# Kernel tuning notes

Hardware: AMD Instinct MI355X
Metric: run time of the kernel (lower is better)

## Reference

```python
import jax, jax.numpy as jnp
import numpy as np

WIN = (4, 16)
HEADS = 4
DIM = 128
HID = 512

def _rel_index(win):
    ch = np.arange(win[0]); cw = np.arange(win[1])
    coords = np.stack(np.meshgrid(ch, cw, indexing='ij')).reshape(2, -1)  # 2, N
    rel = (coords[:, :, None] - coords[:, None, :]).transpose(1, 2, 0).astype(np.int64)  # N,N,2
    rel[:, :, 0] += win[0] - 1
    rel[:, :, 1] += win[1] - 1
    rel[:, :, 0] *= 2 * win[1] - 1
    return jnp.asarray(rel.sum(-1))  # (N, N) int

REL_IDX = _rel_index(WIN)

def _ln(x, g, b):
    m = x.mean(-1, keepdims=True)
    v = ((x - m) ** 2).mean(-1, keepdims=True)
    return (x - m) / jnp.sqrt(v + 1e-5) * g + b

def _gelu(x):
    return jax.nn.gelu(x, approximate=False)

def _posconv3d(x, w, b):
    # depthwise 3x3x3 conv with singleton depth axis; x: B,C,H,W; w: C,1,3,3,3
    y = jax.lax.conv_general_dilated(x[:, :, None], w, (1, 1, 1), ((1, 1), (1, 1), (1, 1)),
                                     feature_group_count=x.shape[1],
                                     dimension_numbers=('NCDHW', 'OIDHW', 'NCDHW'))
    return y[:, :, 0] + b[None, :, None, None]

def _dwconv2d(x, w, b):
    # depthwise 3x3 conv; x: B,Ch,H,W; w: Ch,1,3,3
    y = jax.lax.conv_general_dilated(x, w, (1, 1), ((1, 1), (1, 1)),
                                     feature_group_count=x.shape[1],
                                     dimension_numbers=('NCHW', 'OIHW', 'NCHW'))
    return y + b[None, :, None, None]

def setup_inputs() -> dict:
    key = jax.random.key(0)
    ks = jax.random.split(key, 12)
    B, C, H, W = 4, DIM, 192, 192
    s = 0.02
    return {
        'x': jax.random.normal(ks[0], (B, C, H, W), jnp.float32),
        'pos_w': jax.random.normal(ks[1], (C, 1, 3, 3, 3), jnp.float32) * s,
        'pos_b': jnp.zeros((C,), jnp.float32),
        'ln1_g': jnp.ones((C,), jnp.float32),
        'ln1_b': jnp.zeros((C,), jnp.float32),
        'q_w': jax.random.normal(ks[2], (C, C), jnp.float32) * s,
        'q_b': jnp.zeros((C,), jnp.float32),
        'kv_w': jax.random.normal(ks[3], (C, 2 * C), jnp.float32) * s,
        'kv_b': jnp.zeros((2 * C,), jnp.float32),
        'rpb': jax.random.normal(ks[4], ((2 * WIN[0] - 1) * (2 * WIN[1] - 1), HEADS), jnp.float32) * s,
        'proj_w': jax.random.normal(ks[5], (C, C), jnp.float32) * s,
        'proj_b': jnp.zeros((C,), jnp.float32),
        'fft1_w': jax.random.normal(ks[6], (2 * C, 2 * C), jnp.float32) * s,
        'fft1_b': jnp.zeros((2 * C,), jnp.float32),
        'fft2_w': jax.random.normal(ks[7], (2 * C, 2 * C), jnp.float32) * s,
        'fft2_b': jnp.zeros((2 * C,), jnp.float32),
        'ln2_g': jnp.ones((C,), jnp.float32),
        'ln2_b': jnp.zeros((C,), jnp.float32),
        'l1_w': jax.random.normal(ks[8], (C, HID), jnp.float32) * s,
        'l1_b': jnp.zeros((HID,), jnp.float32),
        'dw_w': jax.random.normal(ks[9], (HID, 1, 3, 3), jnp.float32) * s,
        'dw_b': jnp.zeros((HID,), jnp.float32),
        'l2_w': jax.random.normal(ks[10], (HID, C), jnp.float32) * s,
        'l2_b': jnp.zeros((C,), jnp.float32),
    }

def _forward(x, pos_w, pos_b, ln1_g, ln1_b, q_w, q_b, kv_w, kv_b, rpb, proj_w, proj_b,
             fft1_w, fft1_b, fft2_w, fft2_b, ln2_g, ln2_b, l1_w, l1_b, dw_w, dw_b, l2_w, l2_b):
    B, C, H, W = x.shape
    wh, ww = WIN
    N = wh * ww
    hd = C // HEADS
    # depthwise 3D positional embedding
    x = x + _posconv3d(x, pos_w, pos_b)
    xt = x.transpose(0, 2, 3, 1)  # B,H,W,C
    shortcut = xt
    xn = _ln(xt, ln1_g, ln1_b)
    # window partition: (B*nW, N, C)  (idx=0 -> no shift, no mask)
    win = xn.reshape(B, H // wh, wh, W // ww, ww, C).transpose(0, 1, 3, 2, 4, 5).reshape(-1, N, C)
    q = (win @ q_w + q_b).reshape(-1, N, HEADS, hd).transpose(0, 2, 1, 3)  # Bw,h,N,d
    kv = (win @ kv_w + kv_b).reshape(-1, N, 2, HEADS, hd).transpose(2, 0, 3, 1, 4)
    k, v = kv[0], kv[1]
    attn = jnp.einsum('bhnd,bhmd->bhnm', q * (hd ** -0.5), k)
    rel_bias = rpb[REL_IDX].transpose(2, 0, 1)  # heads,N,N
    attn = jax.nn.softmax(attn + rel_bias[None], axis=-1)
    out = jnp.einsum('bhnm,bhmd->bhnd', attn, v).transpose(0, 2, 1, 3).reshape(-1, N, C)
    out = out @ proj_w + proj_b
    out = out.reshape(B, H // wh, W // ww, wh, ww, C).transpose(0, 1, 3, 2, 4, 5).reshape(B, H, W, C)
    xt = shortcut + out
    # FFT residual branch (two 1x1 convs on cat(real,imag))
    xc = xt.transpose(0, 3, 1, 2)  # B,C,H,W
    f = jnp.fft.rfft2(xc, axes=(-2, -1))
    ff = jnp.concatenate([f.real, f.imag], axis=1)  # B,2C,H,Wf
    ff = jnp.einsum('bchw,co->bohw', ff, fft1_w) + fft1_b[None, :, None, None]
    ff = jnp.where(ff >= 0, ff, 0.01 * ff)  # LeakyReLU(0.01)
    ff = jnp.einsum('bchw,co->bohw', ff, fft2_w) + fft2_b[None, :, None, None]
    fr, fi = jnp.split(ff, 2, axis=1)
    y = jnp.fft.irfft2(fr + 1j * fi, s=(H, W), axes=(-2, -1))
    xt = xt + y.transpose(0, 2, 3, 1)
    # LeFF: linear -> dwconv -> linear, on full (H,W) grid
    xn2 = _ln(xt, ln2_g, ln2_b)
    h1 = _gelu(xn2 @ l1_w + l1_b)               # B,H,W,HID
    h1 = _gelu(_dwconv2d(h1.transpose(0, 3, 1, 2), dw_w, dw_b))
    h2 = h1.transpose(0, 2, 3, 1) @ l2_w + l2_b  # B,H,W,C
    xt = xt + h2
    return xt.transpose(0, 3, 1, 2)

def reference(x, pos_w, pos_b, ln1_g, ln1_b, q_w, q_b, kv_w, kv_b, rpb, proj_w, proj_b,
              fft1_w, fft1_b, fft2_w, fft2_b, ln2_g, ln2_b, l1_w, l1_b, dw_w, dw_b, l2_w, l2_b):
    return _forward(x, pos_w, pos_b, ln1_g, ln1_b, q_w, q_b, kv_w, kv_b, rpb, proj_w, proj_b,
                    fft1_w, fft1_b, fft2_w, fft2_b, ln2_g, ln2_b, l1_w, l1_b, dw_w, dw_b, l2_w, l2_b)
```

## Files before the change

### kernel.cpp

```cpp
#include <hip/hip_runtime.h>
#include <hip/hip_bf16.h>
#include <math.h>

#define C_DIM 128
#define HGT 192
#define WID 192
#define NB 4
#define WFD 97

#define T_BIAS  0
#define T_QKVB  16384
#define TF_SZ   16896
#define UT_MW    0
#define UT_MHF   49152
#define UT_MHI   196608
#define UT_MWI   344064
#define UT_QKVW  387072
#define UT_PROJW 436224
#define UT_FFT1W 452608
#define UT_FFT2W 518144
#define UT_L1W   583680
#define UT_L2W   649216
#define UT_TOT   714752
#define TAB_SZ   374272

typedef __attribute__((ext_vector_type(8))) short bf16x8;
typedef __attribute__((ext_vector_type(4))) float f32x4;

__device__ __forceinline__ float gelu_f(float v){
  return 0.5f*v*(1.0f + erff(v*0.70710678118654752440f));
}
__device__ __forceinline__ unsigned short f2bf(float f){
  __hip_bfloat16 h = __float2bfloat16(f);
  return *reinterpret_cast<unsigned short*>(&h);
}
__device__ __forceinline__ float bf2f(unsigned short u){
  unsigned int x = ((unsigned int)u)<<16;
  return __uint_as_float(x);
}
__device__ __forceinline__ void st8u(unsigned short* d, bf16x8 v){
  unsigned int* wp = (unsigned int*)&v;
  unsigned int* dp = (unsigned int*)d;
  dp[0]=wp[0]; dp[1]=wp[1]; dp[2]=wp[2]; dp[3]=wp[3];
}

__global__ __launch_bounds__(256) void build_tables(float* __restrict__ tab,
        const float* __restrict__ rpb, const float* __restrict__ q_b, const float* __restrict__ kv_b,
        const float* __restrict__ q_w, const float* __restrict__ kv_w, const float* __restrict__ proj_w,
        const float* __restrict__ fft1_w, const float* __restrict__ fft2_w,
        const float* __restrict__ l1_w, const float* __restrict__ l2_w){
  int idx = blockIdx.x*256 + threadIdx.x;
  const float STEP = (float)(6.283185307179586476925286766559/192.0);
  if (idx < 16384){
    int head = idx>>12, n = (idx>>6)&63, m = idx&63;
    int dh = n/16 - m/16 + 3;
    int dw = (n&15) - (m&15) + 15;
    tab[T_BIAS+idx] = rpb[(dh*31+dw)*4 + head];
    return;
  }
  idx -= 16384;
  if (idx < 384){
    tab[T_QKVB+idx] = (idx < 128) ? q_b[idx] : kv_b[idx-128];
    return;
  }
  idx -= 384;
  unsigned short* ut = (unsigned short*)(tab + TF_SZ);
  if (idx < 49152){
    int r = idx/192, w = idx%192;
    float v = 0.f;
    if (r < 97){ int a = (r*w)%192; v = cosf(a*STEP); }
    else if (r < 194){ int a = ((r-97)*w)%192; v = -sinf(a*STEP); }
    ut[UT_MW+idx] = f2bf(v);
    return;
  }
  idx -= 49152;
  if (idx < 147456){
    int r = idx/384, j = idx%384;
    int hf = (r < 192) ? r : r-192;
    int h  = (j < 192) ? j : j-192;
    int a = (hf*h)%192;
    float c = cosf(a*STEP), s = sinf(a*STEP);
    float v;
    if (r < 192) v = (j < 192) ? c : s;
    else         v = (j < 192) ? -s : c;
    ut[UT_MHF+idx] = f2bf(v);
    return;
  }
  idx -= 147456;
  if (idx < 147456){
    int r = idx/384, j = idx%384;
    int h  = (r < 192) ? r : r-192;
    int hf = (j < 192) ? j : j-192;
    int a = (h*hf)%192;
    float c = cosf(a*STEP), s = sinf(a*STEP);
    float v;
    if (r < 192) v = (j < 192) ? c : -s;
    else         v = (j < 192) ? s : c;
    ut[UT_MHI+idx] = f2bf(v);
    return;
  }
  idx -= 147456;
  if (idx < 43008){
    int w = idx/224, j = idx%224;
    float v = 0.f;
    if (j < 97){
      int a = (j*w)%192;
      float sc = ((j==0 || j==96) ? 1.f : 2.f) / 36864.f;
      v = sc*cosf(a*STEP);
    } else if (j >= 112 && j < 209){
      int k = j-112;
      int a = (k*w)%192;
      float sc = ((k==0 || k==96) ? 1.f : 2.f) / 36864.f;
      v = -sc*sinf(a*STEP);
    }
    ut[UT_MWI+idx] = f2bf(v);
    return;
  }
  idx -= 43008;
  if (idx < 49152){
    int n = idx/128, k = idx%128;
    float v = (n < 128) ? q_w[(size_t)k*128 + n] : kv_w[(size_t)k*256 + (n-128)];
    ut[UT_QKVW+idx] = f2bf(v);
    return;
  }
  idx -= 49152;
  if (idx < 16384){
    int n = idx/128, k = idx%128;
    ut[UT_PROJW+idx] = f2bf(proj_w[(size_t)k*128 + n]);
    return;
  }
  idx -= 16384;
  if (idx < 65536){
    int n = idx/256, k = idx%256;
    ut[UT_FFT1W+idx] = f2bf(fft1_w[(size_t)k*256 + n]);
    return;
  }
  idx -= 65536;
  if (idx < 65536){
    int n = idx/256, k = idx%256;
    ut[UT_FFT2W+idx] = f2bf(fft2_w[(size_t)k*256 + n]);
    return;
  }
  idx -= 65536;
  if (idx < 65536){
    int n = idx/128, k = idx%128;
    ut[UT_L1W+idx] = f2bf(l1_w[(size_t)k*512 + n]);
    return;
  }
  idx -= 65536;
  if (idx < 65536){
    int n = idx/512, k = idx%512;
    ut[UT_L2W+idx] = f2bf(l2_w[(size_t)k*128 + n]);
  }
}

__global__ __launch_bounds__(256) void posconv3_kernel(const float* __restrict__ x, const float* __restrict__ pw,
                               const float* __restrict__ pb, float* __restrict__ xt){
  __shared__ float rows_s[16*340];
  int w0 = blockIdx.x*32, h0 = blockIdx.y*8;
  int b = blockIdx.z >> 3, cb = (blockIdx.z & 7)*16;
  int tid = threadIdx.x;
  int hl = tid >> 5, wl = tid & 31;
  for (int e = tid; e < 16*340; e += 256){
    int c = e / 340; int rem = e - c*340;
    int r = rem / 34; int wc = rem - r*34;
    int gh = h0 - 1 + r, gw = w0 - 1 + wc;
    float v = 0.f;
    if (gh >= 0 && gh < HGT && gw >= 0 && gw < WID)
      v = x[((size_t)(b*C_DIM + cb + c))*(HGT*WID) + gh*WID + gw];
    rows_s[e] = v;
  }
  __syncthreads();
  float outr[16];
  #pragma unroll
  for (int c = 0; c < 16; ++c){
    const float* rs = &rows_s[c*340];
    float wreg[9];
    #pragma unroll
    for (int t9 = 0; t9 < 9; ++t9) wreg[t9] = pw[(cb+c)*27 + 9 + t9];
    float bias = pb[cb+c];
    float acc = rs[(hl+1)*34 + wl+1] + bias;
    #pragma unroll
    for (int ky = 0; ky < 3; ++ky)
      #pragma unroll
      for (int kx = 0; kx < 3; ++kx)
        acc += wreg[ky*3+kx]*rs[(hl+ky)*34 + wl+kx];
    outr[c] = acc;
  }
  __syncthreads();
  {
    int px = hl*32 + wl;
    #pragma unroll
    for (int c = 0; c < 16; ++c) rows_s[px*17 + c] = outr[c];
  }
  __syncthreads();
  for (int r = 0; r < 16; ++r){
    int e = r*256 + tid;
    int cl = e & 15, hw = e >> 4;
    int h = hw >> 5, w = hw & 31;
    xt[((size_t)(b*HGT + h0+h)*WID + (w0+w))*C_DIM + cb + cl] = rows_s[hw*17 + cl];
  }
}

__global__ __launch_bounds__(256) void ln_stats_kernel(const float* __restrict__ src, float* __restrict__ stats){
  int wave = threadIdx.x >> 6; int lane = threadIdx.x & 63;
  size_t p = (size_t)blockIdx.x*4 + wave;
  const float* s = src + p*C_DIM;
  float v0 = s[lane], v1 = s[lane+64];
  float sum = v0 + v1;
  #pragma unroll
  for (int o=1; o<64; o<<=1) sum += __shfl_xor(sum, o, 64);
  float m = sum * (1.0f/128.0f);
  float d0 = v0-m, d1 = v1-m;
  float vs = d0*d0 + d1*d1;
  #pragma unroll
  for (int o=1; o<64; o<<=1) vs += __shfl_xor(vs, o, 64);
  float rstd = rsqrtf(vs*(1.0f/128.0f) + 1e-5f);
  if (lane==0){ stats[2*p] = m; stats[2*p+1] = rstd; }
}

template<int ACT, bool ADD, bool LNA, bool ABF, bool OBF, int NT>
__global__ __launch_bounds__(256) void gemm2(const void* __restrict__ A1v,
                            const unsigned short* __restrict__ WT, const float* __restrict__ bias,
                            void* __restrict__ dstv, int K, int N, int lda,
                            const float* __restrict__ stats, const float* __restrict__ lng,
                            const float* __restrict__ lnb, int prow0, int pmax){
  __shared__ __align__(16) unsigned short As[64*40];
  __shared__ __align__(16) unsigned short Bs[NT][64*40];
  int p0 = blockIdx.y*64, n00 = blockIdx.x*(64*NT);
  int tid = threadIdx.x;
  int wave = tid >> 6, lane = tid & 63;
  int wr = (wave>>1)*32, wc = (wave&1)*32;
  f32x4 acc[NT][4];
  #pragma unroll
  for (int nt=0; nt<NT; ++nt)
    #pragma unroll
    for (int q=0; q<4; ++q) acc[nt][q] = (f32x4){};
  int am = tid >> 2, ak = (tid & 3)*8;
  int brow = tid >> 2, bkk = (tid & 3)*8;
  for (int k0 = 0; k0 < K; k0 += 32){
    if constexpr (ABF){
      const unsigned short* A1u = (const unsigned short*)A1v;
      bf16x8 av = *(const bf16x8*)(A1u + (size_t)(p0+am)*lda + k0 + ak);
      st8u(&As[am*40 + ak], av);
    } else {
      int gp = p0 + am;
      float s0 = 0.f, s1 = 0.f;
      if (LNA){
        gp += prow0;
        gp = gp < 0 ? 0 : (gp > pmax ? pmax : gp);
        s0 = stats[2*gp]; s1 = stats[2*gp+1];
      }
      const float* src = (const float*)A1v + (size_t)gp*lda + k0 + ak;
      float4 aa = *(const float4*)src;
      float4 ab = *(const float4*)(src+4);
      float v[8] = {aa.x,aa.y,aa.z,aa.w,ab.x,ab.y,ab.z,ab.w};
      unsigned short* dp = &As[am*40 + ak];
      #pragma unroll
      for (int j=0;j<8;j++){
        float f = v[j];
        if (LNA) f = (f - s0)*s1*lng[k0+ak+j] + lnb[k0+ak+j];
        dp[j] = f2bf(f);
      }
    }
    #pragma unroll
    for (int nt=0; nt<NT; ++nt){
      bf16x8 wv = *(const bf16x8*)(WT + (size_t)(n00 + nt*64 + brow)*K + k0 + bkk);
      st8u(&Bs[nt][brow*40 + bkk], wv);
    }
    __syncthreads();
    int fm = lane & 15, kg = (lane>>4)*8;
    bf16x8 a0 = *(const bf16x8*)&As[(wr+fm)*40 + kg];
    bf16x8 a1 = *(const bf16x8*)&As[(wr+16+fm)*40 + kg];
    #pragma unroll
    for (int nt=0; nt<NT; ++nt){
      bf16x8 b0 = *(const bf16x8*)&Bs[nt][(wc+fm)*40 + kg];
      bf16x8 b1 = *(const bf16x8*)&Bs[nt][(wc+16+fm)*40 + kg];
      acc[nt][0] = __builtin_amdgcn_mfma_f32_16x16x32_bf16(a0, b0, acc[nt][0], 0,0,0);
      acc[nt][1] = __builtin_amdgcn_mfma_f32_16x16x32_bf16(a0, b1, acc[nt][1], 0,0,0);
      acc[nt][2] = __builtin_amdgcn_mfma_f32_16x16x32_bf16(a1, b0, acc[nt][2], 0,0,0);
      acc[nt][3] = __builtin_amdgcn_mfma_f32_16x16x32_bf16(a1, b1, acc[nt][3], 0,0,0);
    }
    __syncthreads();
  }
  int cn = lane & 15, rq = (lane>>4)*4;
  #pragma unroll
  for (int nt=0; nt<NT; ++nt){
    #pragma unroll
    for (int mi=0; mi<2; ++mi){
      #pragma unroll
      for (int ni=0; ni<2; ++ni){
        f32x4 a = acc[nt][mi*2+ni];
        int n = n00 + nt*64 + wc + ni*16 + cn;
        float bsv = bias[n];
        #pragma unroll
        for (int r=0; r<4; ++r){
          size_t row = (size_t)p0 + wr + mi*16 + rq + r;
          float v = a[r] + bsv;
          if (ACT==1) v = (v>=0.f) ? v : 0.01f*v;
          if (ACT==2) v = gelu_f(v);
          if constexpr (OBF){
            ((unsigned short*)dstv)[row*(size_t)N + n] = f2bf(v);
          } else {
            float* dst = (float*)dstv;
            if (ADD) v += dst[row*(size_t)N + n];
            dst[row*(size_t)N + n] = v;
          }
        }
      }
    }
  }
}

template<int MODE>
__global__ __launch_bounds__(256) void dft_gemm(const unsigned short* __restrict__ Atab,
                            const void* __restrict__ W1v, const void* __restrict__ W2v,
                            void* __restrict__ D1v, void* __restrict__ D2v, int k0){
  constexpr int K      = (MODE==0)?192 : (MODE==3)?224 : 384;
  constexpr int MT     = (MODE==0)?4 : (MODE==3)?3 : 6;
  constexpr int MVALID = (MODE==0)?194 : (MODE==3)?192 : 384;
  __shared__ __align__(16) unsigned short As[64*40];
  __shared__ __align__(16) unsigned short Bs[64*40];
  int slab = blockIdx.y / MT;
  int p0 = (blockIdx.y % MT)*64, n0 = blockIdx.x*64;
  int tid = threadIdx.x;
  int wave = tid >> 6, lane = tid & 63;
  int wr = (wave>>1)*32, wc = (wave&1)*32;
  f32x4 acc00 = {}, acc01 = {}, acc10 = {}, acc11 = {};
  int am = tid >> 2, ak = (tid & 3)*8;
  int bk = tid >> 3, bn = (tid & 7)*8;
  for (int kk0 = 0; kk0 < K; kk0 += 32){
    {
      bf16x8 av = *(const bf16x8*)(Atab + (size_t)(p0+am)*K + kk0 + ak);
      st8u(&As[am*40 + ak], av);
    }
    {
      int r = kk0 + bk;
      if (MODE==0){
        const float* src = (const float*)W1v + (size_t)slab*24576 + (size_t)r*128 + n0 + bn;
        float4 wa = *(const float4*)src;
        float4 wb = *(const float4*)(src+4);
        float v[8] = {wa.x,wa.y,wa.z,wa.w,wb.x,wb.y,wb.z,wb.w};
        #pragma unroll
        for (int j=0;j<8;j++) Bs[(bn+j)*40 + bk] = f2bf(v[j]);
      } else {
        const unsigned short* src;
        if (MODE==1) src = (r<192) ? (const unsigned short*)W1v + (size_t)(k0+slab)*128 + (size_t)r*12416
                                   : (const unsigned short*)W2v + (size_t)(k0+slab)*128 + (size_t)(r-192)*12416;
        else if (MODE==2) src = (r<192) ? (const unsigned short*)W1v + (size_t)slab*49152 + (size_t)r*256
                                        : (const unsigned short*)W2v + (size_t)slab*49152 + (size_t)(r-192)*256;
        else src = (r<112) ? (const unsigned short*)W1v + (size_t)slab*24832 + (size_t)r*256
                           : (const unsigned short*)W2v + (size_t)slab*24832 + (size_t)(r-112)*256;
        src += n0 + bn;
        bf16x8 wv = *(const bf16x8*)src;
        #pragma unroll
        for (int j=0;j<8;j++) Bs[(bn+j)*40 + bk] = (unsigned short)wv[j];
      }
    }
    __syncthreads();
    int fm = lane & 15, kg = (lane>>4)*8;
    bf16x8 a0 = *(const bf16x8*)&As[(wr+fm)*40 + kg];
    bf16x8 a1 = *(const bf16x8*)&As[(wr+16+fm)*40 + kg];
    bf16x8 b0 = *(const bf16x8*)&Bs[(wc+fm)*40 + kg];
    bf16x8 b1 = *(const bf16x8*)&Bs[(wc+16+fm)*40 + kg];
    acc00 = __builtin_amdgcn_mfma_f32_16x16x32_bf16(a0, b0, acc00, 0,0,0);
    acc01 = __builtin_amdgcn_mfma_f32_16x16x32_bf16(a0, b1, acc01, 0,0,0);
    acc10 = __builtin_amdgcn_mfma_f32_16x16x32_bf16(a1, b0, acc10, 0,0,0);
    acc11 = __builtin_amdgcn_mfma_f32_16x16x32_bf16(a1, b1, acc11, 0,0,0);
    __syncthreads();
  }
  int cn = lane & 15, rq = (lane>>4)*4;
  #pragma unroll
  for (int mi=0; mi<2; ++mi){
    #pragma unroll
    for (int ni=0; ni<2; ++ni){
      f32x4 a = (mi==0) ? (ni==0?acc00:acc01) : (ni==0?acc10:acc11);
      int n = n0 + wc + ni*16 + cn;
      #pragma unroll
      for (int r=0; r<4; ++r){
        int p = p0 + wr + mi*16 + rq + r;
        if (p >= MVALID) continue;
        float v = a[r];
        if (MODE==0){
          unsigned short* D1 = (unsigned short*)D1v;
          unsigned short* D2 = (unsigned short*)D2v;
          if (p < 97) D1[(size_t)slab*12416 + (size_t)p*128 + n] = f2bf(v);
          else        D2[(size_t)slab*12416 + (size_t)(p-97)*128 + n] = f2bf(v);
        } else if (MODE==1){
          unsigned short* base = (unsigned short*)D1v + (size_t)slab*49152;
          if (p < 192) base[(size_t)p*256 + n] = f2bf(v);
          else         base[(size_t)(p-192)*256 + 128 + n] = f2bf(v);
        } else if (MODE==2){
          unsigned short* D1 = (unsigned short*)D1v;
          int kg2 = k0 + slab;
          if (p < 192) D1[((size_t)p*97 + kg2)*256 + n] = f2bf(v);
          else         D1[((size_t)(p-192)*97 + kg2)*256 + 128 + n] = f2bf(v);
        } else {
          ((float*)D1v)[(size_t)slab*24576 + (size_t)p*128 + n] += v;
        }
      }
    }
  }
}

#define XS_OFF  0
#define WQK_OFF 8704
#define VT_OFF  29184
#define SHM_TOT 38400
__global__ __launch_bounds__(256) void attn_fused2(
    const float* __restrict__ XT, const float* __restrict__ stats,
    const float* __restrict__ g1, const float* __restrict__ b1,
    const unsigned short* __restrict__ QKVW, const float* __restrict__ QKVB,
    const float* __restrict__ biasT, unsigned short* __restrict__ OUTc){
  __shared__ __align__(16) unsigned short shm[SHM_TOT];
  int win = blockIdx.x;
  int b = win/576, rem = win%576, whi = rem/12, wwi = rem%12;
  int tid = threadIdx.x, wave = tid>>6, lane = tid&63, head = wave;
  int fm = lane & 15, kg = (lane>>4)*8;
  size_t rowbase = (size_t)(b*HGT + whi*4)*WID + wwi*16;
  {
    int t = tid >> 2;
    int c0 = (tid & 3)*32;
    size_t grow = rowbase + (size_t)(t>>4)*WID + (t&15);
    const float* src = XT + grow*C_DIM + c0;
    float m = stats[2*grow], rs = stats[2*grow+1];
    unsigned short* dst = &shm[XS_OFF + t*136 + c0];
    #pragma unroll
    for (int j=0;j<32;j++){
      float f = (src[j]-m)*rs*g1[c0+j] + b1[c0+j];
      dst[j] = f2bf(f);
    }
  }
  __syncthreads();
  unsigned short* Qw = &shm[WQK_OFF + wave*5120];
  unsigned short* Kw = Qw + 2560;
  unsigned short* Vt = &shm[VT_OFF + wave*2304];
  #pragma unroll
  for (int op=0; op<3; ++op){
    f32x4 acc[4][2];
    #pragma unroll
    for (int tf=0; tf<4; ++tf){ acc[tf][0] = (f32x4){}; acc[tf][1] = (f32x4){}; }
    int wrow0 = op*128 + head*32;
    #pragma unroll
    for (int kk0=0; kk0<128; kk0+=32){
      bf16x8 bfr0 = *(const bf16x8*)(QKVW + (size_t)(wrow0 + fm)*128 + kk0 + kg);
      bf16x8 bfr1 = *(const bf16x8*)(QKVW + (size_t)(wrow0 + 16 + fm)*128 + kk0 + kg);
      #pragma unroll
      for (int tf=0; tf<4; ++tf){
        bf16x8 af = *(const bf16x8*)&shm[XS_OFF + (tf*16+fm)*136 + kk0 + kg];
        acc[tf][0] = __builtin_amdgcn_mfma_f32_16x16x32_bf16(af, bfr0, acc[tf][0], 0,0,0);
        acc[tf][1] = __builtin_amdgcn_mfma_f32_16x16x32_bf16(af, bfr1, acc[tf][1], 0,0,0);
      }
    }
    #pragma unroll
    for (int tf=0; tf<4; ++tf){
      #pragma unroll
      for (int cf=0; cf<2; ++cf){
        int n = cf*16 + fm;
        float bsv = QKVB[op*128 + head*32 + n];
        #pragma unroll
        for (int r=0;r<4;r++){
          int token = tf*16 + (lane>>4)*4 + r;
          float v = acc[tf][cf][r] + bsv;
          if (op==0) v *= 0.17677669529663688f;
          unsigned short bv = f2bf(v);
          if (op==0)      Qw[token*40 + n] = bv;
          else if (op==1) Kw[token*40 + n] = bv;
          else            Vt[n*72 + token] = bv;
        }
      }
    }
  }
  __syncthreads();
  bf16x8 qf[4], kf[4];
  #pragma unroll
  for (int t4=0; t4<4; ++t4){
    qf[t4] = *(const bf16x8*)&Qw[(t4*16+fm)*40 + kg];
    kf[t4] = *(const bf16x8*)&Kw[(t4*16+fm)*40 + kg];
  }
  f32x4 s[4][4];
  #pragma unroll
  for (int ni=0; ni<4; ++ni)
    #pragma unroll
    for (int mj=0; mj<4; ++mj){
      f32x4 z = {};
      s[ni][mj] = __builtin_amdgcn_mfma_f32_16x16x32_bf16(qf[ni], kf[mj], z, 0,0,0);
    }
  const float* bp = biasT + head*4096;
  #pragma unroll
  for (int ni=0; ni<4; ++ni){
    int nbase = ni*16 + (lane>>4)*4;
    #pragma unroll
    for (int mj=0; mj<4; ++mj){
      int m = mj*16 + fm;
      #pragma unroll
      for (int r=0;r<4;r++)
        s[ni][mj][r] += bp[(nbase+r)*64 + m];
    }
  }
  float rs_[4][4];
  #pragma unroll
  for (int ni=0; ni<4; ++ni){
    #pragma unroll
    for (int r=0;r<4;r++){
      float t = fmaxf(fmaxf(s[ni][0][r], s[ni][1][r]), fmaxf(s[ni][2][r], s[ni][3][r]));
      #pragma unroll
      for (int o=1;o<16;o<<=1) t = fmaxf(t, __shfl_xor(t, o, 64));
      float sum = 0.f;
      #pragma unroll
      for (int mj=0; mj<4; ++mj){
        float e = __expf(s[ni][mj][r] - t);
        s[ni][mj][r] = e;
        sum += e;
      }
      #pragma unroll
      for (int o=1;o<16;o<<=1) sum += __shfl_xor(sum, o, 64);
      rs_[ni][r] = sum;
    }
  }
  __syncthreads();
  unsigned short* Ps = Qw;
  #pragma unroll
  for (int ni=0; ni<4; ++ni){
    int nbase = ni*16 + (lane>>4)*4;
    #pragma unroll
    for (int mj=0; mj<4; ++mj){
      int m = mj*16 + fm;
      #pragma unroll
      for (int r=0;r<4;r++)
        Ps[(nbase+r)*72 + m] = f2bf(s[ni][mj][r]);
    }
  }
  f32x4 o2[4][2];
  #pragma unroll
  for (int ni=0; ni<4; ++ni){ o2[ni][0] = (f32x4){}; o2[ni][1] = (f32x4){}; }
  #pragma unroll
  for (int ks=0; ks<2; ++ks){
    bf16x8 vb0 = *(const bf16x8*)&Vt[fm*72 + ks*32+kg];
    bf16x8 vb1 = *(const bf16x8*)&Vt[(16+fm)*72 + ks*32+kg];
    #pragma unroll
    for (int ni=0; ni<4; ++ni){
      bf16x8 pa = *(const bf16x8*)&Ps[(ni*16+fm)*72 + ks*32+kg];
      o2[ni][0] = __builtin_amdgcn_mfma_f32_16x16x32_bf16(pa, vb0, o2[ni][0], 0,0,0);
      o2[ni][1] = __builtin_amdgcn_mfma_f32_16x16x32_bf16(pa, vb1, o2[ni][1], 0,0,0);
    }
  }
  #pragma unroll
  for (int ni=0; ni<4; ++ni){
    #pragma unroll
    for (int r=0;r<4;r++){
      size_t l = rowbase + (size_t)ni*WID + (lane>>4)*4 + r;
      float inv = 1.0f / rs_[ni][r];
      unsigned short* op = OUTc + l*C_DIM + head*32;
      op[fm]    = f2bf(o2[ni][0][r]*inv);
      op[16+fm] = f2bf(o2[ni][1][r]*inv);
    }
  }
}

__global__ __launch_bounds__(256) void dwconv_strip(const unsigned short* __restrict__ SB1,
                                                    const float* __restrict__ dw,
                                                    const float* __restrict__ db,
                                                    unsigned short* __restrict__ SB2,
                                                    int r0){
  int blk = blockIdx.x;
  int wt = blk % 12, hl = blk / 12;
  int tid = threadIdx.x;
  int c4 = tid & 127, ph = tid >> 7;
  int ch = c4*4;
  int w0 = wt*16 + ph*8;
  int h = r0 + hl;
  float wreg[9][4], bias[4];
  #pragma unroll
  for (int j=0;j<4;j++){
    bias[j] = db[ch+j];
    #pragma unroll
    for (int t9=0;t9<9;t9++) wreg[t9][j] = dw[(ch+j)*9+t9];
  }
  const unsigned short* rp[3];
  bool rv[3];
  #pragma unroll
  for (int ky=0;ky<3;ky++){
    int hh = h + ky - 1;
    rv[ky] = (hh >= 0) && (hh < HGT);
    rp[ky] = SB1 + ((size_t)(hl+ky)*WID)*512 + ch;
  }
  float win[3][3][4];
  #pragma unroll
  for (int ky=0;ky<3;ky++){
    #pragma unroll
    for (int j=0;j<4;j++){ win[ky][0][j]=0.f; win[ky][1][j]=0.f; }
    if (rv[ky]){
      if (w0 > 0){
        const unsigned int* p = (const unsigned int*)(rp[ky] + (size_t)(w0-1)*512);
        unsigned int u0=p[0], u1=p[1];
        win[ky][0][0]=bf2f((unsigned short)(u0&0xFFFF)); win[ky][0][1]=bf2f((unsigned short)(u0>>16));
        win[ky][0][2]=bf2f((unsigned short)(u1&0xFFFF)); win[ky][0][3]=bf2f((unsigned short)(u1>>16));
      }
      {
        const unsigned int* p = (const unsigned int*)(rp[ky] + (size_t)w0*512);
        unsigned int u0=p[0], u1=p[1];
        win[ky][1][0]=bf2f((unsigned short)(u0&0xFFFF)); win[ky][1][1]=bf2f((unsigned short)(u0>>16));
        win[ky][1][2]=bf2f((unsigned short)(u1&0xFFFF)); win[ky][1][3]=bf2f((unsigned short)(u1>>16));
      }
    }
  }
  #pragma unroll
  for (int px=0; px<8; ++px){
    int w = w0 + px;
    #pragma unroll
    for (int ky=0;ky<3;ky++){
      #pragma unroll
      for (int j=0;j<4;j++) win[ky][2][j]=0.f;
      if (rv[ky] && (w+1) < WID){
        const unsigned int* p = (const unsigned int*)(rp[ky] + (size_t)(w+1)*512);
        unsigned int u0=p[0], u1=p[1];
        win[ky][2][0]=bf2f((unsigned short)(u0&0xFFFF)); win[ky][2][1]=bf2f((unsigned short)(u0>>16));
        win[ky][2][2]=bf2f((unsigned short)(u1&0xFFFF)); win[ky][2][3]=bf2f((unsigned short)(u1>>16));
      }
    }
    float a[4];
    #pragma unroll
    for (int j=0;j<4;j++){
      float acc = bias[j];
      #pragma unroll
      for (int ky=0;ky<3;ky++)
        #pragma unroll
        for (int kx=0;kx<3;kx++)
          acc += wreg[ky*3+kx][j]*win[ky][kx][j];
      a[j] = gelu_f(acc);
    }
    unsigned int o0 = (unsigned int)f2bf(a[0]) | ((unsigned int)f2bf(a[1])<<16);
    unsigned int o1 = (unsigned int)f2bf(a[2]) | ((unsigned int)f2bf(a[3])<<16);
    unsigned int* op = (unsigned int*)&SB2[((size_t)hl*WID + w)*512 + ch];
    op[0] = o0; op[1] = o1;
    #pragma unroll
    for (int ky=0;ky<3;ky++)
      #pragma unroll
      for (int j=0;j<4;j++){ win[ky][0][j]=win[ky][1][j]; win[ky][1][j]=win[ky][2][j]; }
  }
}

__global__ __launch_bounds__(256) void transpose_b_kernel(const float* __restrict__ src, float* __restrict__ dst,
                                                          size_t zstride){
  __shared__ float tile[128*65];
  int w0 = blockIdx.x*64, h = blockIdx.y;
  size_t zo = (size_t)blockIdx.z * zstride;
  int tid = threadIdx.x;
  for (int r=0; r<32; r++){
    int e = tid + 256*r; int c = e & 127, wl = e >> 7;
    tile[c*65 + wl] = src[zo + ((size_t)h*WID + w0 + wl)*C_DIM + c];
  }
  __syncthreads();
  for (int r=0; r<32; r++){
    int e = tid + 256*r; int wl = e & 63, c = e >> 6;
    dst[zo + ((size_t)c*HGT + h)*WID + w0 + wl] = tile[c*65 + wl];
  }
}

extern "C" void kernel_launch(void* const* d_in, const int* in_sizes, int n_in,
                              void* d_out, int out_size, void* d_ws, size_t ws_size,
                              hipStream_t stream) {
  const float* x      = (const float*)d_in[0];
  const float* pos_w  = (const float*)d_in[1];
  const float* pos_b  = (const float*)d_in[2];
  const float* ln1_g  = (const float*)d_in[3];
  const float* ln1_b  = (const float*)d_in[4];
  const float* q_w    = (const float*)d_in[5];
  const float* q_b    = (const float*)d_in[6];
  const float* kv_w   = (const float*)d_in[7];
  const float* kv_b   = (const float*)d_in[8];
  const float* rpb    = (const float*)d_in[9];
  const float* proj_w = (const float*)d_in[10];
  const float* proj_b = (const float*)d_in[11];
  const float* fft1_w = (const float*)d_in[12];
  const float* fft1_b = (const float*)d_in[13];
  const float* fft2_w = (const float*)d_in[14];
  const float* fft2_b = (const float*)d_in[15];
  const float* ln2_g  = (const float*)d_in[16];
  const float* ln2_b  = (const float*)d_in[17];
  const float* l1_w   = (const float*)d_in[18];
  const float* l1_b   = (const float*)d_in[19];
  const float* dw_w   = (const float*)d_in[20];
  const float* dw_b   = (const float*)d_in[21];
  const float* l2_w   = (const float*)d_in[22];
  const float* l2_b   = (const float*)d_in[23];

  const size_t S   = (size_t)NB*HGT*WID*C_DIM;
  const size_t Sb  = S/NB;
  const size_t SZb = (size_t)HGT*WFD*C_DIM;
  const size_t GSZ = (size_t)HGT*WFD*256;
  const int    P   = (int)(NB*HGT*WID);

  float* ws    = (float*)d_ws;
  float* TAB   = ws;
  float* STATS = ws + TAB_SZ;
  float* POOL  = ws + TAB_SZ + 2*(size_t)P;
  size_t head  = TAB_SZ + 2*(size_t)P;
  size_t pool  = (ws_size/4 > head) ? (ws_size/4 - head) : 0;

  bool xt_in_pool = (pool >= S + 11000000);
  float* XT     = xt_in_pool ? POOL : (float*)d_out;
  float* POOL2  = xt_in_pool ? POOL + S : POOL;
  size_t pool2  = xt_in_pool ? pool - S : pool;

  const float* biasT = TAB + T_BIAS;
  const float* QKVB  = TAB + T_QKVB;
  const unsigned short* UT = (const unsigned short*)(TAB + TF_SZ);
  const unsigned short* MW  = UT + UT_MW;
  const unsigned short* MHF = UT + UT_MHF;
  const unsigned short* MHI = UT + UT_MHI;
  const unsigned short* MWI = UT + UT_MWI;
  const unsigned short* QKVW  = UT + UT_QKVW;
  const unsigned short* PROJW = UT + UT_PROJW;
  const unsigned short* FFT1W = UT + UT_FFT1W;
  const unsigned short* FFT2W = UT + UT_FFT2W;
  const unsigned short* L1W   = UT + UT_L1W;
  const unsigned short* L2W   = UT + UT_L2W;

  build_tables<<<2858, 256, 0, stream>>>(TAB, rpb, q_b, kv_b, q_w, kv_w, proj_w,
                                         fft1_w, fft2_w, l1_w, l2_w);
  posconv3_kernel<<<dim3(6,24,32), 256, 0, stream>>>(x, pos_w, pos_b, XT);

  ln_stats_kernel<<<P/4, 256, 0, stream>>>(XT, STATS);
  {
    unsigned short* OUTu = (unsigned short*)POOL2;
    attn_fused2<<<2304, 256, 0, stream>>>(XT, STATS, ln1_g, ln1_b, QKVW, QKVB, biasT, OUTu);
    gemm2<0,true,false,true,false,2><<<dim3(1, P/64), 256, 0, stream>>>(
        OUTu, PROJW, proj_b, XT, 128, 128, 128, nullptr, nullptr, nullptr, 0, 0);
  }

  {
    unsigned short* FRu = (unsigned short*)POOL2;
    unsigned short* FIu = FRu + SZb;
    unsigned short* Gu  = FIu + SZb;
    size_t fixed = SZb + GSZ/2;
    int CKmax = 1;
    if (pool2 > fixed + 49152) CKmax = (int)((pool2 - fixed)/49152);
    if (CKmax < 1) CKmax = 1;
    if (CKmax > WFD) CKmax = WFD;
    int nch = (WFD + CKmax - 1)/CKmax;
    int CK = (WFD + nch - 1)/nch;
    unsigned short* FF0u = (unsigned short*)(POOL2 + fixed);
    unsigned short* FF1u = FF0u + (size_t)CK*49152;
    for (int b = 0; b < NB; ++b){
      float* XTb = XT + (size_t)b*Sb;
      dft_gemm<0><<<dim3(2, 192*4), 256, 0, stream>>>(MW, XTb, nullptr, FRu, FIu, 0);
      for (int k0 = 0; k0 < WFD; k0 += CK){
        int ck = (WFD - k0 < CK) ? (WFD - k0) : CK;
        int rows = ck*192;
        dft_gemm<1><<<dim3(2, ck*6), 256, 0, stream>>>(MHF, FRu, FIu, FF0u, nullptr, k0);
        gemm2<1,false,false,true,true,1><<<dim3(4, rows/64), 256, 0, stream>>>(
            FF0u, FFT1W, fft1_b, FF1u, 256, 256, 256, nullptr, nullptr, nullptr, 0, 0);
        gemm2<0,false,false,true,true,1><<<dim3(4, rows/64), 256, 0, stream>>>(
            FF1u, FFT2W, fft2_b, FF0u, 256, 256, 256, nullptr, nullptr, nullptr, 0, 0);
        dft_gemm<2><<<dim3(2, ck*6), 256, 0, stream>>>(MHI, FF0u, FF0u+128, Gu, nullptr, k0);
      }
      dft_gemm<3><<<dim3(2, 192*3), 256, 0, stream>>>(MWI, Gu, Gu+128, XTb, nullptr, 0);
    }
  }

  ln_stats_kernel<<<P/4, 256, 0, stream>>>(XT, STATS);

  {
    int SH = 96;
    while ((size_t)(3*SH+4)*49152 > pool2 && SH > 24) SH >>= 1;
    const size_t SB1SZ = (size_t)(SH+2)*98304;
    unsigned short* SB1u[2] = { (unsigned short*)POOL2, (unsigned short*)POOL2 + SB1SZ };
    unsigned short* SB2u = (unsigned short*)POOL2 + 2*SB1SZ;
    int nStrips = HGT/SH;
    for (int b = 0; b < NB; ++b){
      auto launch_g = [&](int s){
        int r0 = s*SH;
        int prow0 = (b*HGT + r0 - 1)*WID;
        gemm2<2,false,true,false,true,2><<<dim3(4, (SH+2)*3), 256, 0, stream>>>(
            XT, L1W, l1_b, SB1u[s&1], 128, 512, 128,
            STATS, ln2_g, ln2_b, prow0, P-1);
      };
      launch_g(0);
      for (int s = 0; s < nStrips; ++s){
        if (s+1 < nStrips) launch_g(s+1);
        int r0 = s*SH;
        dwconv_strip<<<12*SH, 256, 0, stream>>>(SB1u[s&1], dw_w, dw_b, SB2u, r0);
        gemm2<0,true,false,true,false,1><<<dim3(2, SH*3), 256, 0, stream>>>(
            SB2u, L2W, l2_b, XT + ((size_t)(b*HGT + r0)*WID)*C_DIM,
            512, 128, 512, nullptr, nullptr, nullptr, 0, 0);
      }
    }
  }

  if (xt_in_pool){
    transpose_b_kernel<<<dim3(3,192,4), 256, 0, stream>>>(XT, (float*)d_out, Sb);
  } else {
    for (int b = 0; b < NB; ++b){
      transpose_b_kernel<<<dim3(3,192,1), 256, 0, stream>>>(XT + (size_t)b*Sb, POOL2, 0);
      hipMemcpyAsync((float*)d_out + (size_t)b*Sb, POOL2, Sb*sizeof(float),
                     hipMemcpyDeviceToDevice, stream);
    }
  }
}
```

Before: 1.184 ms.

## Fuse attention output projection and residual add into windowed attention kernel

The attention kernel now writes its per-window output into shared memory instead of a global bf16 buffer. After a barrier, each wave runs the 128x128 projection GEMM with MFMA and adds the result plus bias straight into XT as the residual. This drops the separate projection GEMM launch and the global round trip of the attention output. In exchange the attention kernel uses more registers and does a read-modify-write on XT, whose stores from this layout may coalesce less well.

```diff
diff --git a/kernel.cpp b/kernel.cpp
--- a/kernel.cpp
+++ b/kernel.cpp
@@ -407,11 +407,12 @@
 #define WQK_OFF 8704
 #define VT_OFF  29184
 #define SHM_TOT 38400
-__global__ __launch_bounds__(256) void attn_fused2(
-    const float* __restrict__ XT, const float* __restrict__ stats,
+__global__ __launch_bounds__(256) void attn_fused3(
+    float* __restrict__ XT, const float* __restrict__ stats,
     const float* __restrict__ g1, const float* __restrict__ b1,
     const unsigned short* __restrict__ QKVW, const float* __restrict__ QKVB,
-    const float* __restrict__ biasT, unsigned short* __restrict__ OUTc){
+    const float* __restrict__ biasT, const unsigned short* __restrict__ PROJW,
+    const float* __restrict__ projb){
   __shared__ __align__(16) unsigned short shm[SHM_TOT];
   int win = blockIdx.x;
   int b = win/576, rem = win%576, whi = rem/12, wwi = rem%12;
@@ -549,11 +550,42 @@
   for (int ni=0; ni<4; ++ni){
     #pragma unroll
     for (int r=0;r<4;r++){
-      size_t l = rowbase + (size_t)ni*WID + (lane>>4)*4 + r;
+      int token = ni*16 + (lane>>4)*4 + r;
       float inv = 1.0f / rs_[ni][r];
-      unsigned short* op = OUTc + l*C_DIM + head*32;
+      unsigned short* op = &shm[XS_OFF + token*136 + head*32];
       op[fm]    = f2bf(o2[ni][0][r]*inv);
       op[16+fm] = f2bf(o2[ni][1][r]*inv);
+    }
+  }
+  __syncthreads();
+  {
+    f32x4 pacc[4][2];
+    #pragma unroll
+    for (int tf=0; tf<4; ++tf){ pacc[tf][0] = (f32x4){}; pacc[tf][1] = (f32x4){}; }
+    int wrow0 = wave*32;
+    #pragma unroll
+    for (int kk0=0; kk0<128; kk0+=32){
+      bf16x8 bfr0 = *(const bf16x8*)(PROJW + (size_t)(wrow0 + fm)*128 + kk0 + kg);
+      bf16x8 bfr1 = *(const bf16x8*)(PROJW + (size_t)(wrow0 + 16 + fm)*128 + kk0 + kg);
+      #pragma unroll
+      for (int tf=0; tf<4; ++tf){
+        bf16x8 af = *(const bf16x8*)&shm[XS_OFF + (tf*16+fm)*136 + kk0 + kg];
+        pacc[tf][0] = __builtin_amdgcn_mfma_f32_16x16x32_bf16(af, bfr0, pacc[tf][0], 0,0,0);
+        pacc[tf][1] = __builtin_amdgcn_mfma_f32_16x16x32_bf16(af, bfr1, pacc[tf][1], 0,0,0);
+      }
+    }
+    #pragma unroll
+    for (int tf=0; tf<4; ++tf){
+      #pragma unroll
+      for (int cf=0; cf<2; ++cf){
+        int n = wave*32 + cf*16 + fm;
+        float bsv = projb[n];
+        #pragma unroll
+        for (int r=0;r<4;r++){
+          size_t l = rowbase + (size_t)tf*WID + (lane>>4)*4 + r;
+          XT[l*C_DIM + n] += pacc[tf][cf][r] + bsv;
+        }
+      }
     }
   }
 }
@@ -723,12 +755,8 @@
   posconv3_kernel<<<dim3(6,24,32), 256, 0, stream>>>(x, pos_w, pos_b, XT);
 
   ln_stats_kernel<<<P/4, 256, 0, stream>>>(XT, STATS);
-  {
-    unsigned short* OUTu = (unsigned short*)POOL2;
-    attn_fused2<<<2304, 256, 0, stream>>>(XT, STATS, ln1_g, ln1_b, QKVW, QKVB, biasT, OUTu);
-    gemm2<0,true,false,true,false,2><<<dim3(1, P/64), 256, 0, stream>>>(
-        OUTu, PROJW, proj_b, XT, 128, 128, 128, nullptr, nullptr, nullptr, 0, 0);
-  }
+  attn_fused3<<<2304, 256, 0, stream>>>(XT, STATS, ln1_g, ln1_b, QKVW, QKVB,
+                                        biasT, PROJW, proj_b);
 
   {
     unsigned short* FRu = (unsigned short*)POOL2;
```

Measured after the change: 1.153 ms. 2.5% less time.
